# Kernel tuning notes

Measured on AMD Instinct MI355X. Metric: run time of the kernel, lower is better.

Reference implementation:

```python
import jax, jax.numpy as jnp
import numpy as np

N_NODES = 50000
N_EDGES = 800000
IN_F = 128
HEADS = 4
OUT_F = 16  # per-head channels; concat output = HEADS*OUT_F = 64
NEG_SLOPE = 0.2


def setup_inputs() -> dict:
    key = jax.random.key(0)
    ks = jax.random.split(key, 9)
    x = jax.random.normal(ks[0], (N_NODES, IN_F), dtype=jnp.float32)
    edge_index = jax.random.randint(ks[1], (2, N_EDGES), 0, N_NODES, dtype=jnp.int64)
    edge_attr = jax.random.normal(ks[2], (N_EDGES, 1), dtype=jnp.float32)
    s = 1.0 / np.sqrt(IN_F)
    W = jax.random.normal(ks[3], (IN_F, HEADS * OUT_F), dtype=jnp.float32) * s
    W_edge = jax.random.normal(ks[4], (1, HEADS * OUT_F), dtype=jnp.float32)
    att_src = jax.random.normal(ks[5], (HEADS, OUT_F), dtype=jnp.float32) * s
    att_dst = jax.random.normal(ks[6], (HEADS, OUT_F), dtype=jnp.float32) * s
    att_edge = jax.random.normal(ks[7], (HEADS, OUT_F), dtype=jnp.float32) * s
    bias = jax.random.normal(ks[8], (HEADS * OUT_F,), dtype=jnp.float32) * 0.01
    return {"x": x, "edge_index": edge_index, "edge_attr": edge_attr,
            "W": W, "W_edge": W_edge, "att_src": att_src,
            "att_dst": att_dst, "att_edge": att_edge, "bias": bias}


def reference(x, edge_index, edge_attr, W, W_edge, att_src, att_dst, att_edge, bias):
    N = x.shape[0]
    H, C = att_src.shape
    src, dst = edge_index[0], edge_index[1]

    # add_self_loops with fill_value='mean': per-dst mean of incoming edge_attr
    deg = jax.ops.segment_sum(jnp.ones_like(edge_attr[:, 0]), dst, num_segments=N)
    ea_mean = jax.ops.segment_sum(edge_attr, dst, num_segments=N) / jnp.maximum(deg, 1.0)[:, None]
    loop = jnp.arange(N, dtype=src.dtype)
    src_f = jnp.concatenate([src, loop])   # [E+N]
    dst_f = jnp.concatenate([dst, loop])
    ea = jnp.concatenate([edge_attr, ea_mean], axis=0)  # [E+N, 1]

    # node transform + per-node attention logits
    xw = (x @ W).reshape(N, H, C)                 # [N,H,C]
    a_src = jnp.einsum('nhc,hc->nh', xw, att_src)  # [N,H]
    a_dst = jnp.einsum('nhc,hc->nh', xw, att_dst)

    # edge feature transform + edge logits
    ew = (ea @ W_edge).reshape(-1, H, C)           # [E+N,H,C]
    a_edge = jnp.einsum('ehc,hc->eh', ew, att_edge)

    # gather, LeakyReLU, segment softmax over incoming edges per dst node
    alpha = jax.nn.leaky_relu(a_src[src_f] + a_dst[dst_f] + a_edge, NEG_SLOPE)  # [E+N,H]
    amax = jax.ops.segment_max(alpha, dst_f, num_segments=N)                    # [N,H]
    ex = jnp.exp(alpha - amax[dst_f])
    denom = jax.ops.segment_sum(ex, dst_f, num_segments=N)
    att = ex / denom[dst_f]                                                     # [E+N,H]

    # weighted scatter-aggregate of source messages
    msg = xw[src_f] * att[:, :, None]                       # [E+N,H,C]
    out = jax.ops.segment_sum(msg, dst_f, num_segments=N)    # [N,H,C]
    out = out.reshape(N, H * C) + bias

    # batchnorm=Identity, dropout in eval mode; activation=relu
    return jax.nn.relu(out)
```

## Files before the change

kernel.cpp:

```cpp
#include <hip/hip_runtime.h>
#include <hip/hip_fp16.h>
#include <math.h>

#define NN 50000
#define NE 800000
#define INF_ 128
#define HEADS 4
#define OUTF 16
#define HC 64
#define NEG_SLOPE 0.2f
#define NBKT 196
#define CHA 4096
#define NBA ((NE + CHA - 1) / CHA)
#define WPB 4

__device__ __forceinline__ unsigned short h2u(float f) {
    __half h = __float2half(f);
    return *(unsigned short*)&h;
}
__device__ __forceinline__ float u2f(unsigned short u) {
    __half h = *(__half*)&u;
    return __half2float(h);
}

__global__ __launch_bounds__(256) void k_xw(
    const float* __restrict__ x, const float* __restrict__ W,
    const float* __restrict__ att_src, const float* __restrict__ att_dst,
    unsigned short* __restrict__ xw16, unsigned short* __restrict__ a_src16,
    float* __restrict__ a_dst) {
    __shared__ float sW[INF_ * HC];
    __shared__ float sx[64 * 132];
    int t = threadIdx.x;
    int n0 = blockIdx.x * 64;
    for (int i = t; i < (INF_ * HC) / 4; i += 256)
        ((float4*)sW)[i] = ((const float4*)W)[i];
    for (int i = t; i < 64 * 32; i += 256) {
        int r = i >> 5, k4 = (i & 31) * 4;
        int n = n0 + r;
        float4 v = (n < NN) ? *(const float4*)&x[(size_t)n * INF_ + k4]
                            : make_float4(0.f, 0.f, 0.f, 0.f);
        *(float4*)&sx[r * 132 + k4] = v;
    }
    __syncthreads();
    int cg = t & 15;
    int q  = t >> 4;
    int c0 = cg * 4;
    float acc[4][4];
#pragma unroll
    for (int j = 0; j < 4; ++j)
#pragma unroll
        for (int i = 0; i < 4; ++i) acc[j][i] = 0.f;
#pragma unroll 4
    for (int k = 0; k < INF_; ++k) {
        float4 w = *(const float4*)&sW[k * HC + c0];
#pragma unroll
        for (int j = 0; j < 4; ++j) {
            float xv = sx[(q * 4 + j) * 132 + k];
            acc[j][0] = fmaf(xv, w.x, acc[j][0]);
            acc[j][1] = fmaf(xv, w.y, acc[j][1]);
            acc[j][2] = fmaf(xv, w.z, acc[j][2]);
            acc[j][3] = fmaf(xv, w.w, acc[j][3]);
        }
    }
    int h = c0 >> 4;
    int cl = c0 & 15;
    float ps[4], pd[4];
#pragma unroll
    for (int j = 0; j < 4; ++j) {
        float s_ = 0.f, d_ = 0.f;
#pragma unroll
        for (int i = 0; i < 4; ++i) {
            s_ = fmaf(acc[j][i], att_src[h * OUTF + cl + i], s_);
            d_ = fmaf(acc[j][i], att_dst[h * OUTF + cl + i], d_);
        }
        ps[j] = s_; pd[j] = d_;
    }
#pragma unroll
    for (int m = 1; m < 4; m <<= 1)
#pragma unroll
        for (int j = 0; j < 4; ++j) {
            ps[j] += __shfl_xor(ps[j], m);
            pd[j] += __shfl_xor(pd[j], m);
        }
#pragma unroll
    for (int j = 0; j < 4; ++j) {
        int n = n0 + q * 4 + j;
        if (n < NN) {
            ushort4 u;
            u.x = h2u(acc[j][0]); u.y = h2u(acc[j][1]);
            u.z = h2u(acc[j][2]); u.w = h2u(acc[j][3]);
            *(ushort4*)&xw16[(size_t)n * HC + c0] = u;
            if ((cg & 3) == 0) {
                a_src16[n * HEADS + h] = h2u(ps[j]);
                a_dst[n * HEADS + h] = pd[j];
            }
        }
    }
}

__global__ __launch_bounds__(256) void k_coarse(const int* __restrict__ ei,
                                                int* __restrict__ ccnt) {
    __shared__ int lh[NBKT];
    int t = threadIdx.x;
    for (int i = t; i < NBKT; i += 256) lh[i] = 0;
    __syncthreads();
    for (int i = blockIdx.x * 256 + t; i < NE; i += gridDim.x * 256)
        atomicAdd(&lh[ei[NE + i] >> 8], 1);
    __syncthreads();
    for (int i = t; i < NBKT; i += 256)
        if (lh[i]) atomicAdd(&ccnt[i], lh[i]);
}

__global__ void k_scanb(const int* __restrict__ ccnt, int* __restrict__ boff,
                        int* __restrict__ ccur) {
    __shared__ int sd[256];
    int t = threadIdx.x;
    int v = (t < NBKT) ? ccnt[t] : 0;
    sd[t] = v; __syncthreads();
    for (int o = 1; o < 256; o <<= 1) {
        int a = (t >= o) ? sd[t - o] : 0;
        __syncthreads();
        sd[t] += a;
        __syncthreads();
    }
    int ex = sd[t] - v;
    if (t < NBKT) { boff[t] = ex; ccur[t] = ex; }
    if (t == NBKT - 1) boff[NBKT] = sd[t];
}

__global__ __launch_bounds__(256) void k_binA(const int* __restrict__ ei,
                                              const float* __restrict__ ea,
                                              int* __restrict__ ccur,
                                              uint2* __restrict__ ebuf) {
    __shared__ int lh[NBKT], lcur[NBKT];
    int t = threadIdx.x;
    int e0 = blockIdx.x * CHA;
    int ecnt = NE - e0; if (ecnt > CHA) ecnt = CHA;
    for (int i = t; i < NBKT; i += 256) lh[i] = 0;
    __syncthreads();
    for (int i = t; i < ecnt; i += 256)
        atomicAdd(&lh[ei[NE + e0 + i] >> 8], 1);
    __syncthreads();
    for (int i = t; i < NBKT; i += 256)
        lcur[i] = lh[i] ? atomicAdd(&ccur[i], lh[i]) : 0;
    __syncthreads();
    for (int i = t; i < ecnt; i += 256) {
        int e = e0 + i;
        int dst = ei[NE + e];
        int b = dst >> 8;
        int p = atomicAdd(&lcur[b], 1);
        uint2 pk;
        pk.x = (unsigned)ei[e] | ((unsigned)(dst & 255) << 16);
        pk.y = __float_as_uint(ea[e]);
        ebuf[p] = pk;
    }
}

__global__ __launch_bounds__(256) void k_binB(const int* __restrict__ boff,
                                              const uint2* __restrict__ ebuf,
                                              uint2* __restrict__ esort,
                                              int* __restrict__ deg,
                                              int* __restrict__ offs) {
    __shared__ int lh[256], lo_[256], lcur[256], sd[256];
    int t = threadIdx.x;
    int b = blockIdx.x;
    int base = boff[b];
    int cnt = boff[b + 1] - base;
    lh[t] = 0;
    __syncthreads();
    for (int i = t; i < cnt; i += 256)
        atomicAdd(&lh[(ebuf[base + i].x >> 16) & 255], 1);
    __syncthreads();
    int v = lh[t];
    sd[t] = v; __syncthreads();
    for (int o = 1; o < 256; o <<= 1) {
        int a = (t >= o) ? sd[t - o] : 0;
        __syncthreads();
        sd[t] += a;
        __syncthreads();
    }
    int ex = sd[t] - v;
    lo_[t] = ex; lcur[t] = ex;
    __syncthreads();
    for (int i = t; i < cnt; i += 256) {
        uint2 pk = ebuf[base + i];
        int d = (pk.x >> 16) & 255;
        int p = atomicAdd(&lcur[d], 1);
        esort[base + p] = make_uint2(pk.x & 0xFFFFu, pk.y);
    }
    int n = (b << 8) + t;
    if (n < NN) { deg[n] = v; offs[n] = base + ex; }
}

__device__ __forceinline__ float sel4s(float a, float b, float c, float d, int h) {
    float ab = (h & 1) ? b : a;
    float cd = (h & 1) ? d : c;
    return (h & 2) ? cd : ab;
}
__device__ __forceinline__ float lrelu(float v) {
    return v > 0.f ? v : NEG_SLOPE * v;
}

__global__ __launch_bounds__(256) void k_gather(
    const uint2* __restrict__ esort, const int* __restrict__ offs,
    const int* __restrict__ deg,
    const unsigned short* __restrict__ a_src16, const float* __restrict__ a_dst,
    const unsigned short* __restrict__ xw16,
    const float* __restrict__ W_edge, const float* __restrict__ att_edge,
    const float* __restrict__ bias, float* __restrict__ out) {
    __shared__ __align__(16) float sce[4];
    __shared__ __align__(16) float ldsP[WPB][64][4];
    __shared__ int ldsS[WPB][64];
    int t = threadIdx.x;
    if (t < 4) {
        float s_ = 0.f;
        for (int k = 0; k < OUTF; ++k)
            s_ = fmaf(W_edge[t * OUTF + k], att_edge[t * OUTF + k], s_);
        sce[t] = s_;
    }
    __syncthreads();
    int lane = t & 63;
    int wslot = t >> 6;
    int n = (blockIdx.x << 2) + wslot;
    int hc = lane >> 4;

    float4 ce4 = *(float4*)sce;
    float4 ad4 = *(const float4*)&a_dst[(size_t)n * 4];
    int start = offs[n];
    int cnt = deg[n];

    float m0 = -3e38f, m1 = -3e38f, m2 = -3e38f, m3 = -3e38f;
    float s = 0.f, acc = 0.f, easum = 0.f;

    int nch = (cnt + 63) >> 6;
    for (int ch = 0; ch < nch; ++ch) {
        int base = start + (ch << 6);
        int cc = cnt - (ch << 6); if (cc > 64) cc = 64;
        bool valid = lane < cc;
        float l0, l1, l2, l3, eav = 0.f; int srci = 0;
        if (valid) {
            uint2 pk = esort[base + lane];
            srci = (int)pk.x;
            eav = __uint_as_float(pk.y);
            uint2 au = *(const uint2*)&a_src16[(size_t)srci * 4];
            float as0 = u2f((unsigned short)(au.x & 0xFFFF));
            float as1 = u2f((unsigned short)(au.x >> 16));
            float as2 = u2f((unsigned short)(au.y & 0xFFFF));
            float as3 = u2f((unsigned short)(au.y >> 16));
            l0 = lrelu(as0 + ad4.x + eav * ce4.x);
            l1 = lrelu(as1 + ad4.y + eav * ce4.y);
            l2 = lrelu(as2 + ad4.z + eav * ce4.z);
            l3 = lrelu(as3 + ad4.w + eav * ce4.w);
        } else {
            l0 = l1 = l2 = l3 = -3e38f;
        }
        float es = valid ? eav : 0.f;
#pragma unroll
        for (int mm = 1; mm < 64; mm <<= 1) es += __shfl_xor(es, mm);
        easum += es;
        float c0 = l0, c1 = l1, c2 = l2, c3 = l3;
#pragma unroll
        for (int mm = 1; mm < 64; mm <<= 1) {
            c0 = fmaxf(c0, __shfl_xor(c0, mm));
            c1 = fmaxf(c1, __shfl_xor(c1, mm));
            c2 = fmaxf(c2, __shfl_xor(c2, mm));
            c3 = fmaxf(c3, __shfl_xor(c3, mm));
        }
        float n0 = fmaxf(m0, c0), n1 = fmaxf(m1, c1);
        float n2 = fmaxf(m2, c2), n3 = fmaxf(m3, c3);
        float mo = sel4s(m0, m1, m2, m3, hc);
        float mn = sel4s(n0, n1, n2, n3, hc);
        float r = __expf(mo - mn);
        s *= r; acc *= r;
        if (valid) {
            float4 pv4;
            pv4.x = __expf(l0 - n0);
            pv4.y = __expf(l1 - n1);
            pv4.z = __expf(l2 - n2);
            pv4.w = __expf(l3 - n3);
            *(float4*)&ldsP[wslot][lane][0] = pv4;
            ldsS[wslot][lane] = srci;
        }
        m0 = n0; m1 = n1; m2 = n2; m3 = n3;
        asm volatile("s_waitcnt lgkmcnt(0)" ::: "memory");
        __builtin_amdgcn_sched_barrier(0);
#pragma unroll 4
        for (int i = 0; i < cc; ++i) {
            float pv = ldsP[wslot][i][hc];
            int si = ldsS[wslot][i];
            float xv = u2f(xw16[(size_t)si * HC + lane]);
            s += pv;
            acc = fmaf(pv, xv, acc);
        }
        asm volatile("s_waitcnt lgkmcnt(0)" ::: "memory");
        __builtin_amdgcn_sched_barrier(0);
    }
    uint2 au = *(const uint2*)&a_src16[(size_t)n * 4];
    float ss0 = u2f((unsigned short)(au.x & 0xFFFF));
    float ss1 = u2f((unsigned short)(au.x >> 16));
    float ss2 = u2f((unsigned short)(au.y & 0xFFFF));
    float ss3 = u2f((unsigned short)(au.y >> 16));
    float asn = sel4s(ss0, ss1, ss2, ss3, hc);
    float adn = sel4s(ad4.x, ad4.y, ad4.z, ad4.w, hc);
    float cen = sel4s(ce4.x, ce4.y, ce4.z, ce4.w, hc);
    float mown = sel4s(m0, m1, m2, m3, hc);
    float eavm = easum / fmaxf((float)cnt, 1.f);
    float al = lrelu(asn + adn + eavm * cen);
    float mn = fmaxf(mown, al);
    float r = __expf(mown - mn);
    float p = __expf(al - mn);
    float xself = u2f(xw16[(size_t)n * HC + lane]);
    s = s * r + p;
    acc = acc * r + p * xself;
    out[(size_t)n * HC + lane] = fmaxf(acc / s + bias[lane], 0.f);
}

extern "C" void kernel_launch(void* const* d_in, const int* in_sizes, int n_in,
                              void* d_out, int out_size, void* d_ws, size_t ws_size,
                              hipStream_t stream) {
    const float* x        = (const float*)d_in[0];
    const int*   ei       = (const int*)d_in[1];
    const float* ea       = (const float*)d_in[2];
    const float* W        = (const float*)d_in[3];
    const float* W_edge   = (const float*)d_in[4];
    const float* att_src  = (const float*)d_in[5];
    const float* att_dst  = (const float*)d_in[6];
    const float* att_edge = (const float*)d_in[7];
    const float* bias     = (const float*)d_in[8];
    float* out = (float*)d_out;

    float* ws = (float*)d_ws;
    unsigned short* xw16    = (unsigned short*)ws;
    uint2* esort  = (uint2*)(ws + (size_t)32 * NN);
    uint2* ebuf   = esort + NE;
    unsigned short* a_src16 = (unsigned short*)(ebuf + NE);
    float* a_dst  = (float*)(a_src16 + (size_t)HEADS * NN);
    int*   deg    = (int*)(a_dst + (size_t)HEADS * NN);
    int*   offs   = deg + NN;
    int*   ccnt   = offs + NN;
    int*   ccur   = ccnt + NBKT;
    int*   boff   = ccur + NBKT;

    hipMemsetAsync(ccnt, 0, NBKT * sizeof(int), stream);
    k_coarse<<<256, 256, 0, stream>>>(ei, ccnt);
    k_scanb<<<1, 256, 0, stream>>>(ccnt, boff, ccur);
    k_binA<<<NBA, 256, 0, stream>>>(ei, ea, ccur, ebuf);
    k_binB<<<NBKT, 256, 0, stream>>>(boff, ebuf, esort, deg, offs);
    k_xw<<<(NN + 63) / 64, 256, 0, stream>>>(x, W, att_src, att_dst, xw16, a_src16, a_dst);
    k_gather<<<NN / 4, 256, 0, stream>>>(
        esort, offs, deg, a_src16, a_dst, xw16, W_edge, att_edge, bias, out);
}
```

Measured before the change: 191.1 us.

## Use fp16 MFMA for node transform and 16-edge head-split chunks in gather

The node-feature GEMM now runs on MFMA 16x16x32 fp16 instructions. x and a transposed W are converted to half in LDS, and the attention dot products are reduced with 16-lane shuffles. The gather kernel processes edges in chunks of 16, with each 16-lane group handling one head. This drops the four-way per-lane logit computation and the 64-wide shuffle reductions, at the cost of more chunk iterations for high-degree nodes. Rounding the GEMM inputs to fp16 reduces accuracy. Loads of esort past the valid count are now unguarded.

```diff
diff --git a/kernel.cpp b/kernel.cpp
--- a/kernel.cpp
+++ b/kernel.cpp
@@ -13,6 +13,10 @@
 #define CHA 4096
 #define NBA ((NE + CHA - 1) / CHA)
 #define WPB 4
+#define XPAD 136
+
+typedef _Float16 half8 __attribute__((ext_vector_type(8)));
+typedef float f32x4 __attribute__((ext_vector_type(4)));
 
 __device__ __forceinline__ unsigned short h2u(float f) {
     __half h = __float2half(f);
@@ -28,71 +32,66 @@
     const float* __restrict__ att_src, const float* __restrict__ att_dst,
     unsigned short* __restrict__ xw16, unsigned short* __restrict__ a_src16,
     float* __restrict__ a_dst) {
-    __shared__ float sW[INF_ * HC];
-    __shared__ float sx[64 * 132];
+    __shared__ _Float16 sxh[64][XPAD];
+    __shared__ _Float16 sWT[64][XPAD];
     int t = threadIdx.x;
     int n0 = blockIdx.x * 64;
-    for (int i = t; i < (INF_ * HC) / 4; i += 256)
-        ((float4*)sW)[i] = ((const float4*)W)[i];
     for (int i = t; i < 64 * 32; i += 256) {
-        int r = i >> 5, k4 = (i & 31) * 4;
+        int r = i >> 5, c4 = (i & 31) * 4;
         int n = n0 + r;
-        float4 v = (n < NN) ? *(const float4*)&x[(size_t)n * INF_ + k4]
+        float4 v = (n < NN) ? *(const float4*)&x[(size_t)n * INF_ + c4]
                             : make_float4(0.f, 0.f, 0.f, 0.f);
-        *(float4*)&sx[r * 132 + k4] = v;
-    }
-    __syncthreads();
-    int cg = t & 15;
-    int q  = t >> 4;
-    int c0 = cg * 4;
-    float acc[4][4];
-#pragma unroll
-    for (int j = 0; j < 4; ++j)
-#pragma unroll
-        for (int i = 0; i < 4; ++i) acc[j][i] = 0.f;
-#pragma unroll 4
-    for (int k = 0; k < INF_; ++k) {
-        float4 w = *(const float4*)&sW[k * HC + c0];
+        sxh[r][c4 + 0] = (_Float16)v.x;
+        sxh[r][c4 + 1] = (_Float16)v.y;
+        sxh[r][c4 + 2] = (_Float16)v.z;
+        sxh[r][c4 + 3] = (_Float16)v.w;
+    }
+    for (int i = t; i < INF_ * HC; i += 256) {
+        int k = i >> 6, c = i & 63;
+        sWT[c][k] = (_Float16)W[i];
+    }
+    __syncthreads();
+    int w = t >> 6, l = t & 63;
+    int lr = l & 15, kg = l >> 4;
+    f32x4 acc0 = {0.f,0.f,0.f,0.f}, acc1 = acc0, acc2 = acc0, acc3 = acc0;
+#pragma unroll
+    for (int kk = 0; kk < 4; ++kk) {
+        half8 a = *(half8*)&sxh[w * 16 + lr][kk * 32 + kg * 8];
+        half8 b0 = *(half8*)&sWT[0 * 16 + lr][kk * 32 + kg * 8];
+        half8 b1 = *(half8*)&sWT[1 * 16 + lr][kk * 32 + kg * 8];
+        half8 b2 = *(half8*)&sWT[2 * 16 + lr][kk * 32 + kg * 8];
+        half8 b3 = *(half8*)&sWT[3 * 16 + lr][kk * 32 + kg * 8];
+        acc0 = __builtin_amdgcn_mfma_f32_16x16x32_f16(a, b0, acc0, 0, 0, 0);
+        acc1 = __builtin_amdgcn_mfma_f32_16x16x32_f16(a, b1, acc1, 0, 0, 0);
+        acc2 = __builtin_amdgcn_mfma_f32_16x16x32_f16(a, b2, acc2, 0, 0, 0);
+        acc3 = __builtin_amdgcn_mfma_f32_16x16x32_f16(a, b3, acc3, 0, 0, 0);
+    }
+    float attS[4], attD[4];
+#pragma unroll
+    for (int ct = 0; ct < 4; ++ct) {
+        attS[ct] = att_src[ct * 16 + lr];
+        attD[ct] = att_dst[ct * 16 + lr];
+    }
+    int rbase = n0 + w * 16 + kg * 4;
+    f32x4 accs[4] = {acc0, acc1, acc2, acc3};
+#pragma unroll
+    for (int ct = 0; ct < 4; ++ct) {
 #pragma unroll
         for (int j = 0; j < 4; ++j) {
-            float xv = sx[(q * 4 + j) * 132 + k];
-            acc[j][0] = fmaf(xv, w.x, acc[j][0]);
-            acc[j][1] = fmaf(xv, w.y, acc[j][1]);
-            acc[j][2] = fmaf(xv, w.z, acc[j][2]);
-            acc[j][3] = fmaf(xv, w.w, acc[j][3]);
-        }
-    }
-    int h = c0 >> 4;
-    int cl = c0 & 15;
-    float ps[4], pd[4];
-#pragma unroll
-    for (int j = 0; j < 4; ++j) {
-        float s_ = 0.f, d_ = 0.f;
-#pragma unroll
-        for (int i = 0; i < 4; ++i) {
-            s_ = fmaf(acc[j][i], att_src[h * OUTF + cl + i], s_);
-            d_ = fmaf(acc[j][i], att_dst[h * OUTF + cl + i], d_);
-        }
-        ps[j] = s_; pd[j] = d_;
-    }
-#pragma unroll
-    for (int m = 1; m < 4; m <<= 1)
-#pragma unroll
-        for (int j = 0; j < 4; ++j) {
-            ps[j] += __shfl_xor(ps[j], m);
-            pd[j] += __shfl_xor(pd[j], m);
-        }
-#pragma unroll
-    for (int j = 0; j < 4; ++j) {
-        int n = n0 + q * 4 + j;
-        if (n < NN) {
-            ushort4 u;
-            u.x = h2u(acc[j][0]); u.y = h2u(acc[j][1]);
-            u.z = h2u(acc[j][2]); u.w = h2u(acc[j][3]);
-            *(ushort4*)&xw16[(size_t)n * HC + c0] = u;
-            if ((cg & 3) == 0) {
-                a_src16[n * HEADS + h] = h2u(ps[j]);
-                a_dst[n * HEADS + h] = pd[j];
+            float c = accs[ct][j];
+            int node = rbase + j;
+            if (node < NN)
+                xw16[(size_t)node * HC + ct * 16 + lr] = h2u(c);
+            float vs = c * attS[ct];
+            float vd = c * attD[ct];
+#pragma unroll
+            for (int m = 1; m < 16; m <<= 1) {
+                vs += __shfl_xor(vs, m);
+                vd += __shfl_xor(vd, m);
+            }
+            if (lr == 0 && node < NN) {
+                a_src16[node * HEADS + ct] = h2u(vs);
+                a_dst[node * HEADS + ct] = vd;
             }
         }
     }
@@ -161,7 +160,7 @@
                                               uint2* __restrict__ esort,
                                               int* __restrict__ deg,
                                               int* __restrict__ offs) {
-    __shared__ int lh[256], lo_[256], lcur[256], sd[256];
+    __shared__ int lh[256], lcur[256], sd[256];
     int t = threadIdx.x;
     int b = blockIdx.x;
     int base = boff[b];
@@ -180,7 +179,7 @@
         __syncthreads();
     }
     int ex = sd[t] - v;
-    lo_[t] = ex; lcur[t] = ex;
+    lcur[t] = ex;
     __syncthreads();
     for (int i = t; i < cnt; i += 256) {
         uint2 pk = ebuf[base + i];
@@ -192,11 +191,6 @@
     if (n < NN) { deg[n] = v; offs[n] = base + ex; }
 }
 
-__device__ __forceinline__ float sel4s(float a, float b, float c, float d, int h) {
-    float ab = (h & 1) ? b : a;
-    float cd = (h & 1) ? d : c;
-    return (h & 2) ? cd : ab;
-}
 __device__ __forceinline__ float lrelu(float v) {
     return v > 0.f ? v : NEG_SLOPE * v;
 }
@@ -209,8 +203,8 @@
     const float* __restrict__ W_edge, const float* __restrict__ att_edge,
     const float* __restrict__ bias, float* __restrict__ out) {
     __shared__ __align__(16) float sce[4];
-    __shared__ __align__(16) float ldsP[WPB][64][4];
-    __shared__ int ldsS[WPB][64];
+    __shared__ __align__(16) float ldsP[WPB][16][4];
+    __shared__ int ldsS[WPB][16];
     int t = threadIdx.x;
     if (t < 4) {
         float s_ = 0.f;
@@ -222,71 +216,49 @@
     int lane = t & 63;
     int wslot = t >> 6;
     int n = (blockIdx.x << 2) + wslot;
-    int hc = lane >> 4;
-
-    float4 ce4 = *(float4*)sce;
-    float4 ad4 = *(const float4*)&a_dst[(size_t)n * 4];
+    int e16 = lane & 15;
+    int h = lane >> 4;
+
+    float ceh = sce[h];
+    float adh = a_dst[n * HEADS + h];
     int start = offs[n];
     int cnt = deg[n];
 
-    float m0 = -3e38f, m1 = -3e38f, m2 = -3e38f, m3 = -3e38f;
-    float s = 0.f, acc = 0.f, easum = 0.f;
-
-    int nch = (cnt + 63) >> 6;
+    float m = -3e38f, s = 0.f, acc = 0.f, easum = 0.f;
+
+    int nch = (cnt + 15) >> 4;
     for (int ch = 0; ch < nch; ++ch) {
-        int base = start + (ch << 6);
-        int cc = cnt - (ch << 6); if (cc > 64) cc = 64;
-        bool valid = lane < cc;
-        float l0, l1, l2, l3, eav = 0.f; int srci = 0;
-        if (valid) {
-            uint2 pk = esort[base + lane];
-            srci = (int)pk.x;
-            eav = __uint_as_float(pk.y);
-            uint2 au = *(const uint2*)&a_src16[(size_t)srci * 4];
-            float as0 = u2f((unsigned short)(au.x & 0xFFFF));
-            float as1 = u2f((unsigned short)(au.x >> 16));
-            float as2 = u2f((unsigned short)(au.y & 0xFFFF));
-            float as3 = u2f((unsigned short)(au.y >> 16));
-            l0 = lrelu(as0 + ad4.x + eav * ce4.x);
-            l1 = lrelu(as1 + ad4.y + eav * ce4.y);
-            l2 = lrelu(as2 + ad4.z + eav * ce4.z);
-            l3 = lrelu(as3 + ad4.w + eav * ce4.w);
-        } else {
-            l0 = l1 = l2 = l3 = -3e38f;
+        int base = start + (ch << 4);
+        int cc = cnt - (ch << 4); if (cc > 16) cc = 16;
+        bool valid = e16 < cc;
+        uint2 pk = esort[base + e16];
+        int srci = (int)(pk.x & 0xFFFFu);
+        float eav = valid ? __uint_as_float(pk.y) : 0.f;
+        float lg = -3e38f;
+        {
+            float asv = u2f(a_src16[srci * HEADS + h]);
+            float v = asv + adh + eav * ceh;
+            if (valid) lg = lrelu(v);
         }
-        float es = valid ? eav : 0.f;
-#pragma unroll
-        for (int mm = 1; mm < 64; mm <<= 1) es += __shfl_xor(es, mm);
+        float es = eav;
+#pragma unroll
+        for (int mm = 1; mm < 16; mm <<= 1) es += __shfl_xor(es, mm);
         easum += es;
-        float c0 = l0, c1 = l1, c2 = l2, c3 = l3;
-#pragma unroll
-        for (int mm = 1; mm < 64; mm <<= 1) {
-            c0 = fmaxf(c0, __shfl_xor(c0, mm));
-            c1 = fmaxf(c1, __shfl_xor(c1, mm));
-            c2 = fmaxf(c2, __shfl_xor(c2, mm));
-            c3 = fmaxf(c3, __shfl_xor(c3, mm));
-        }
-        float n0 = fmaxf(m0, c0), n1 = fmaxf(m1, c1);
-        float n2 = fmaxf(m2, c2), n3 = fmaxf(m3, c3);
-        float mo = sel4s(m0, m1, m2, m3, hc);
-        float mn = sel4s(n0, n1, n2, n3, hc);
-        float r = __expf(mo - mn);
+        float cm = lg;
+#pragma unroll
+        for (int mm = 1; mm < 16; mm <<= 1) cm = fmaxf(cm, __shfl_xor(cm, mm));
+        float nh = fmaxf(m, cm);
+        float r = __expf(m - nh);
         s *= r; acc *= r;
-        if (valid) {
-            float4 pv4;
-            pv4.x = __expf(l0 - n0);
-            pv4.y = __expf(l1 - n1);
-            pv4.z = __expf(l2 - n2);
-            pv4.w = __expf(l3 - n3);
-            *(float4*)&ldsP[wslot][lane][0] = pv4;
-            ldsS[wslot][lane] = srci;
-        }
-        m0 = n0; m1 = n1; m2 = n2; m3 = n3;
+        m = nh;
+        float p = __expf(lg - nh);
+        ldsP[wslot][e16][h] = p;
+        if (h == 0) ldsS[wslot][e16] = srci;
         asm volatile("s_waitcnt lgkmcnt(0)" ::: "memory");
         __builtin_amdgcn_sched_barrier(0);
 #pragma unroll 4
         for (int i = 0; i < cc; ++i) {
-            float pv = ldsP[wslot][i][hc];
+            float pv = ldsP[wslot][i][h];
             int si = ldsS[wslot][i];
             float xv = u2f(xw16[(size_t)si * HC + lane]);
             s += pv;
@@ -295,19 +267,11 @@
         asm volatile("s_waitcnt lgkmcnt(0)" ::: "memory");
         __builtin_amdgcn_sched_barrier(0);
     }
-    uint2 au = *(const uint2*)&a_src16[(size_t)n * 4];
-    float ss0 = u2f((unsigned short)(au.x & 0xFFFF));
-    float ss1 = u2f((unsigned short)(au.x >> 16));
-    float ss2 = u2f((unsigned short)(au.y & 0xFFFF));
-    float ss3 = u2f((unsigned short)(au.y >> 16));
-    float asn = sel4s(ss0, ss1, ss2, ss3, hc);
-    float adn = sel4s(ad4.x, ad4.y, ad4.z, ad4.w, hc);
-    float cen = sel4s(ce4.x, ce4.y, ce4.z, ce4.w, hc);
-    float mown = sel4s(m0, m1, m2, m3, hc);
+    float asn = u2f(a_src16[n * HEADS + h]);
     float eavm = easum / fmaxf((float)cnt, 1.f);
-    float al = lrelu(asn + adn + eavm * cen);
-    float mn = fmaxf(mown, al);
-    float r = __expf(mown - mn);
+    float al = lrelu(asn + adh + eavm * ceh);
+    float mn = fmaxf(m, al);
+    float r = __expf(m - mn);
     float p = __expf(al - mn);
     float xself = u2f(xw16[(size_t)n * HC + lane]);
     s = s * r + p;
```

Result: faster. 184.7 us (-3.4%).
